# Kernel tuning notes

Hardware: AMD Instinct MI355X
Metric: run time of the kernel (lower is better)

## Reference

```python
import jax, jax.numpy as jnp
import numpy as np

RADIUS = 1.0


def setup_inputs() -> dict:
    key = jax.random.key(0)
    ks = jax.random.split(key, 9)
    Nq, No, P, L = 1024, 2048, 3, 64
    pos_query = jax.random.uniform(ks[0], (Nq, P), dtype=jnp.float32)
    pos_obs = jax.random.uniform(ks[1], (No, P), dtype=jnp.float32)
    h_obs = jax.random.normal(ks[2], (No, L), dtype=jnp.float32)
    # kernel_mlp: Linear(3*P, L) -> ReLU -> Linear(L, 1)
    W1 = jax.random.normal(ks[3], (3 * P, L), dtype=jnp.float32) * (1.0 / np.sqrt(3 * P))
    b1 = jnp.zeros((L,), jnp.float32)
    W2 = jax.random.normal(ks[4], (L, 1), dtype=jnp.float32) * (1.0 / np.sqrt(L))
    b2 = jnp.zeros((1,), jnp.float32)
    # value_proj: Linear(L, L)
    Wv = jax.random.normal(ks[5], (L, L), dtype=jnp.float32) * (1.0 / np.sqrt(L))
    bv = jnp.zeros((L,), jnp.float32)
    obs_mask = jnp.ones((No,), jnp.int32)
    obs_batch = jnp.sort(jax.random.randint(ks[6], (No,), 0, 4, dtype=jnp.int32))
    query_batch = jnp.sort(jax.random.randint(ks[7], (Nq,), 0, 4, dtype=jnp.int32))
    return dict(h_obs=h_obs, pos_obs=pos_obs, pos_query=pos_query,
                W1=W1, b1=b1, W2=W2, b2=b2, Wv=Wv, bv=bv,
                obs_mask=obs_mask, obs_batch=obs_batch, query_batch=query_batch)


def reference(h_obs, pos_obs, pos_query, W1, b1, W2, b2, Wv, bv,
              obs_mask, obs_batch, query_batch):
    Nq, P = pos_query.shape
    No = pos_obs.shape[0]
    rel = pos_query[:, None, :] - pos_obs[None, :, :]                 # [Nq,No,P]
    kin = jnp.concatenate([
        jnp.broadcast_to(pos_query[:, None, :], (Nq, No, P)),
        jnp.broadcast_to(pos_obs[None, :, :], (Nq, No, P)),
        rel,
    ], axis=-1)                                                        # [Nq,No,3P]
    hidden = jax.nn.relu(jnp.einsum('qop,pl->qol', kin, W1) + b1)      # [Nq,No,L]
    logits = jnp.einsum('qol,lk->qok', hidden, W2)[..., 0] + b2[0]     # [Nq,No]
    # masks: same batch, within radius, observed
    same = query_batch[:, None] == obs_batch[None, :]
    dist = jnp.linalg.norm(rel, axis=-1)
    mask = same & (dist <= RADIUS) & (obs_mask[None, :] != 0)
    # masked softmax over obs dim; fully-masked rows -> all-zero weights
    # (matches torch softmax(-inf row) -> nan -> nan_to_num(0))
    logits_safe = jnp.where(mask, logits, 0.0)
    m = jnp.max(jnp.where(mask, logits, -jnp.inf), axis=1, keepdims=True)
    m = jnp.where(jnp.isfinite(m), m, 0.0)
    e = jnp.where(mask, jnp.exp(logits_safe - m), 0.0)
    denom = jnp.sum(e, axis=1, keepdims=True)
    weights = e / jnp.maximum(denom, 1e-30)                            # [Nq,No]
    v = h_obs @ Wv + bv                                                # [No,L]
    return weights @ v                                                 # [Nq,L]
```

## Files before the change

### kernel.cpp

```cpp
#include <hip/hip_runtime.h>
#include <math.h>

#define LDIM 64
#define QT2 32
#define QW 8
#define QT3 4
#define SEG 4
#define LOG2E 1.4426950408889634f

static __device__ __forceinline__ float fast_exp2(float x) {
#if __has_builtin(__builtin_amdgcn_exp2f)
    return __builtin_amdgcn_exp2f(x);
#else
    return exp2f(x);
#endif
}

__global__ __launch_bounds__(256) void gano_pre(
    const float* __restrict__ h_obs, const float* __restrict__ pos_obs,
    const float* __restrict__ pos_query,
    const float* __restrict__ W1, const float* __restrict__ b1,
    const float* __restrict__ W2,
    const float* __restrict__ Wv, const float* __restrict__ bv,
    const int* __restrict__ obs_mask, const int* __restrict__ obs_batch,
    const int* __restrict__ query_batch,
    float4* __restrict__ Bi, float4* __restrict__ P4,
    float* __restrict__ V, float* __restrict__ A, float* __restrict__ w2s,
    int2* __restrict__ qrange,
    int No, int NoA, int Nq)
{
    const int gid = blockIdx.x * blockDim.x + threadIdx.x;
    if (gid >= NoA * LDIM) return;
    {
        const int o = gid >> 6, l = gid & 63;
        float vv = 0.0f;
        if (o < No) {
            vv = bv[l];
            #pragma unroll 8
            for (int k = 0; k < LDIM; ++k)
                vv = fmaf(h_obs[o * LDIM + k], Wv[k * LDIM + l], vv);
        }
        V[gid] = vv;
    }
    if (gid < NoA * 16) {
        const int o = gid & 63, g = (gid >> 6) & 15, c = gid >> 10;
        const int oo = (c << 6) + o;
        float4 r = make_float4(0.f, 0.f, 0.f, 0.f);
        if (oo < No) {
            const float px = pos_obs[oo*3+0], py = pos_obs[oo*3+1], pz = pos_obs[oo*3+2];
            float* rr = (float*)&r;
            #pragma unroll
            for (int j = 0; j < 4; ++j) {
                const int l = 4 * g + j;
                float bb = b1[l];
                bb = fmaf(px, W1[3*LDIM+l] - W1[6*LDIM+l], bb);
                bb = fmaf(py, W1[4*LDIM+l] - W1[7*LDIM+l], bb);
                bb = fmaf(pz, W1[5*LDIM+l] - W1[8*LDIM+l], bb);
                rr[j] = bb;
            }
        }
        Bi[gid] = r;
    }
    if (gid < Nq * LDIM) {
        const int q = gid >> 6, l = gid & 63;
        float a = pos_query[q*3+0] * (W1[0*LDIM+l] + W1[6*LDIM+l]);
        a = fmaf(pos_query[q*3+1], W1[1*LDIM+l] + W1[7*LDIM+l], a);
        a = fmaf(pos_query[q*3+2], W1[2*LDIM+l] + W1[8*LDIM+l], a);
        A[gid] = a;
    }
    if (gid < LDIM) w2s[gid] = W2[gid] * LOG2E;
    if (gid < NoA) {
        float4 pp = make_float4(0.f, 0.f, 0.f, 0.f);
        if (gid < No)
            pp = make_float4(pos_obs[gid*3+0], pos_obs[gid*3+1], pos_obs[gid*3+2],
                             obs_mask[gid] ? (float)(obs_batch[gid] + 1) : 0.0f);
        P4[gid] = pp;
    }
    if (gid < Nq) {
        const int b = query_batch[gid];
        int lo = 0, hi = No;
        while (lo < hi) { int mid = (lo + hi) >> 1; if (obs_batch[mid] < b) lo = mid + 1; else hi = mid; }
        const int s = lo;
        hi = No;
        while (lo < hi) { int mid = (lo + hi) >> 1; if (obs_batch[mid] < b + 1) lo = mid + 1; else hi = mid; }
        qrange[gid] = make_int2(s, lo);
    }
}

__global__ __launch_bounds__(256) void gano_logits(
    const float4* __restrict__ Bi, const float4* __restrict__ P4,
    const float* __restrict__ A, const float* __restrict__ w2s,
    const float* __restrict__ pos_query,
    const int* __restrict__ obs_batch, const int* __restrict__ query_batch,
    float* __restrict__ lg, int No, int NoA)
{
    const int c  = blockIdx.x;
    const int q0 = blockIdx.y * QT2;
    if ((c << 6) >= No) return;
    const int c_lo = obs_batch[c << 6];
    const int c_hi = obs_batch[min((c << 6) + 63, No - 1)];
    const int t_lo = query_batch[q0];
    const int t_hi = query_batch[q0 + QT2 - 1];
    if (c_lo > t_hi || c_hi < t_lo) return;

    __shared__ float4 a4[QT2][16];
    __shared__ float4 w2_4[16];
    __shared__ float4 qp4[QT2];

    const int tid = threadIdx.x;
    for (int i = tid; i < QT2 * 16; i += 256)
        a4[i >> 4][i & 15] = ((const float4*)A)[((size_t)(q0 + (i >> 4)) << 4) + (i & 15)];
    if (tid < 16) w2_4[tid] = ((const float4*)w2s)[tid];
    if (tid < QT2) {
        const int q = q0 + tid;
        qp4[tid] = make_float4(pos_query[q*3+0], pos_query[q*3+1], pos_query[q*3+2],
                               (float)(query_batch[q] + 1));
    }
    __syncthreads();

    const int lane = tid & 63, wid = tid >> 6;
    const float4 p = P4[(c << 6) + lane];
    const float4* Bc = Bi + ((size_t)c << 10) + lane;

    float lgq[QW];
    #pragma unroll
    for (int j = 0; j < QW; ++j) lgq[j] = 0.0f;

    #pragma unroll
    for (int g = 0; g < 16; ++g) {
        const float4 Bv = Bc[g << 6];
        const float4 w  = w2_4[g];
        #pragma unroll
        for (int j = 0; j < QW; ++j) {
            const float4 a = a4[wid * QW + j][g];
            lgq[j] = fmaf(fmaxf(a.x + Bv.x, 0.f), w.x, lgq[j]);
            lgq[j] = fmaf(fmaxf(a.y + Bv.y, 0.f), w.y, lgq[j]);
            lgq[j] = fmaf(fmaxf(a.z + Bv.z, 0.f), w.z, lgq[j]);
            lgq[j] = fmaf(fmaxf(a.w + Bv.w, 0.f), w.w, lgq[j]);
        }
    }

    float* lrow = lg + (size_t)(q0 + wid * QW) * NoA + (c << 6) + lane;
    #pragma unroll
    for (int j = 0; j < QW; ++j) {
        const float4 qp = qp4[wid * QW + j];
        const float dx = qp.x - p.x, dy = qp.y - p.y, dz = qp.z - p.z;
        const float d2 = fmaf(dz, dz, fmaf(dy, dy, dx * dx));
        const bool valid = (p.w == qp.w) & (d2 <= 1.0f);
        lrow[(size_t)j * NoA] = valid ? lgq[j] : -INFINITY;
    }
}

__global__ __launch_bounds__(256) void gano_pv(
    const float* __restrict__ lg, const float* __restrict__ V,
    const int2* __restrict__ qrange,
    float* __restrict__ partA, int NoA)
{
    const int grp = blockIdx.x >> 2;
    const int seg = blockIdx.x & 3;
    const int q0  = grp * QT3;
    const int tid = threadIdx.x, lane = tid & 63, wid = tid >> 6;

    __shared__ float sM[QT3], sD[QT3];
    __shared__ float4 e4[4][LDIM];
    __shared__ float sacc[4][QT3][LDIM];

    {
        const int q = q0 + wid;
        const int2 r = qrange[q];
        const float* row = lg + (size_t)q * NoA;
        float mx = -INFINITY;
        for (int o = r.x + lane; o < r.y; o += 64) mx = fmaxf(mx, row[o]);
        #pragma unroll
        for (int m = 32; m; m >>= 1) mx = fmaxf(mx, __shfl_xor(mx, m, 64));
        const float Mq = (mx == -INFINITY) ? 0.0f : mx;
        float sum = 0.0f;
        for (int o = r.x + lane; o < r.y; o += 64) sum += fast_exp2(row[o] - Mq);
        #pragma unroll
        for (int m = 32; m; m >>= 1) sum += __shfl_xor(sum, m, 64);
        if (lane == 0) { sM[wid] = Mq; sD[wid] = sum; }
    }
    __syncthreads();

    const float M0 = sM[0], M1 = sM[1], M2 = sM[2], M3 = sM[3];
    float acc0 = 0.f, acc1 = 0.f, acc2 = 0.f, acc3 = 0.f;

    const int s4 = qrange[q0].x;
    const int e4u = qrange[q0 + QT3 - 1].y;
    if (e4u > s4) {
        const int c0 = s4 >> 6, c1 = (e4u - 1) >> 6;
        const int nc = c1 - c0 + 1;
        const int cs = c0 + (nc * seg) / SEG;
        const int ce = c0 + (nc * (seg + 1)) / SEG;
        const float* r0 = lg + (size_t)(q0 + 0) * NoA;
        const float* r1 = lg + (size_t)(q0 + 1) * NoA;
        const float* r2 = lg + (size_t)(q0 + 2) * NoA;
        const float* r3 = lg + (size_t)(q0 + 3) * NoA;
        for (int c = cs + wid; c < ce; c += 4) {
            const int o = (c << 6) + lane;
            float4 ev;
            ev.x = fast_exp2(r0[o] - M0);
            ev.y = fast_exp2(r1[o] - M1);
            ev.z = fast_exp2(r2[o] - M2);
            ev.w = fast_exp2(r3[o] - M3);
            e4[wid][lane] = ev;
            const float* Vc = V + ((size_t)c << 12) + lane;
            #pragma unroll
            for (int oo = 0; oo < LDIM; ++oo) {
                const float4 e = e4[wid][oo];
                const float vv = Vc[oo << 6];
                acc0 = fmaf(e.x, vv, acc0);
                acc1 = fmaf(e.y, vv, acc1);
                acc2 = fmaf(e.z, vv, acc2);
                acc3 = fmaf(e.w, vv, acc3);
            }
        }
    }

    sacc[wid][0][lane] = acc0;
    sacc[wid][1][lane] = acc1;
    sacc[wid][2][lane] = acc2;
    sacc[wid][3][lane] = acc3;
    __syncthreads();

    {
        const int q = wid;
        const float a = (sacc[0][q][lane] + sacc[1][q][lane]) +
                        (sacc[2][q][lane] + sacc[3][q][lane]);
        const float rd = 1.0f / fmaxf(sD[q], 1e-30f);
        partA[(((size_t)(q0 + q)) * SEG + seg) * LDIM + lane] = a * rd;
    }
}

__global__ __launch_bounds__(256) void gano_merge(
    const float* __restrict__ partA, float* __restrict__ out, int n)
{
    const int gid = blockIdx.x * blockDim.x + threadIdx.x;
    if (gid >= n) return;
    const int q = gid >> 6, l = gid & 63;
    const float* p = partA + ((size_t)q * SEG) * LDIM + l;
    out[gid] = (p[0] + p[LDIM]) + (p[2 * LDIM] + p[3 * LDIM]);
}

extern "C" void kernel_launch(void* const* d_in, const int* in_sizes, int n_in,
                              void* d_out, int out_size, void* d_ws, size_t ws_size,
                              hipStream_t stream) {
    const float* h_obs     = (const float*)d_in[0];
    const float* pos_obs   = (const float*)d_in[1];
    const float* pos_query = (const float*)d_in[2];
    const float* W1        = (const float*)d_in[3];
    const float* b1        = (const float*)d_in[4];
    const float* W2        = (const float*)d_in[5];
    const float* Wv        = (const float*)d_in[7];
    const float* bv        = (const float*)d_in[8];
    const int* obs_mask    = (const int*)d_in[9];
    const int* obs_batch   = (const int*)d_in[10];
    const int* query_batch = (const int*)d_in[11];

    const int No  = in_sizes[1] / 3;
    const int Nq  = in_sizes[2] / 3;
    const int NoA = (No + 63) & ~63;
    const int nChunks = NoA / 64;

    float4* Bi  = (float4*)d_ws;
    float4* P4  = Bi + (size_t)NoA * 16;
    float*  V   = (float*)(P4 + NoA);
    float*  A   = V + (size_t)NoA * LDIM;
    float*  w2s = A + (size_t)Nq * LDIM;
    int2*   qr  = (int2*)(w2s + LDIM);
    float*  lgb = (float*)(qr + Nq);
    float*  pA  = lgb + (size_t)Nq * NoA;

    gano_pre<<<(NoA * LDIM + 255) / 256, 256, 0, stream>>>(
        h_obs, pos_obs, pos_query, W1, b1, W2, Wv, bv,
        obs_mask, obs_batch, query_batch,
        Bi, P4, V, A, w2s, qr, No, NoA, Nq);

    dim3 g2(nChunks, Nq / QT2);
    gano_logits<<<g2, 256, 0, stream>>>(Bi, P4, A, w2s, pos_query,
                                        obs_batch, query_batch, lgb, No, NoA);

    gano_pv<<<(Nq / QT3) * SEG, 256, 0, stream>>>(lgb, V, qr, pA, NoA);

    gano_merge<<<(Nq * LDIM + 255) / 256, 256, 0, stream>>>(pA, (float*)d_out, Nq * LDIM);
}
```

Baseline: 31.87 us.

## Compute per-chunk softmax max/sum in logits kernel and drop merge pass

The logits kernel now applies the mask, then computes a per-64-obs-chunk max and exp-sum for each query with wave shuffles. It stores the exponentials plus those chunk statistics instead of raw logits. The PV kernel merges the chunk statistics into a row max and denominator, and rescales the stored exponentials by a per-chunk factor. This removes the two full-row passes for max and sum and the separate merge kernel launch. In exchange, the 4-way segment split of PV is dropped, so far fewer blocks run, and the combine step assumes at most 64 chunks per query group.

```diff
diff --git a/kernel.cpp b/kernel.cpp
--- a/kernel.cpp
+++ b/kernel.cpp
@@ -5,7 +5,6 @@
 #define QT2 32
 #define QW 8
 #define QT3 4
-#define SEG 4
 #define LOG2E 1.4426950408889634f
 
 static __device__ __forceinline__ float fast_exp2(float x) {
@@ -92,16 +91,15 @@
     const float* __restrict__ A, const float* __restrict__ w2s,
     const float* __restrict__ pos_query,
     const int* __restrict__ obs_batch, const int* __restrict__ query_batch,
-    float* __restrict__ lg, int No, int NoA)
+    float* __restrict__ ec, float* __restrict__ cmax, float* __restrict__ csum,
+    int No, int NoA, int nC)
 {
     const int c  = blockIdx.x;
     const int q0 = blockIdx.y * QT2;
     if ((c << 6) >= No) return;
     const int c_lo = obs_batch[c << 6];
     const int c_hi = obs_batch[min((c << 6) + 63, No - 1)];
-    const int t_lo = query_batch[q0];
-    const int t_hi = query_batch[q0 + QT2 - 1];
-    if (c_lo > t_hi || c_hi < t_lo) return;
+    if (c_lo > query_batch[q0 + QT2 - 1] || c_hi < query_batch[q0]) return;
 
     __shared__ float4 a4[QT2][16];
     __shared__ float4 w2_4[16];
@@ -140,70 +138,102 @@
         }
     }
 
-    float* lrow = lg + (size_t)(q0 + wid * QW) * NoA + (c << 6) + lane;
     #pragma unroll
     for (int j = 0; j < QW; ++j) {
         const float4 qp = qp4[wid * QW + j];
         const float dx = qp.x - p.x, dy = qp.y - p.y, dz = qp.z - p.z;
         const float d2 = fmaf(dz, dz, fmaf(dy, dy, dx * dx));
         const bool valid = (p.w == qp.w) & (d2 <= 1.0f);
-        lrow[(size_t)j * NoA] = valid ? lgq[j] : -INFINITY;
+        lgq[j] = valid ? lgq[j] : -INFINITY;
+    }
+
+    float mc[QW];
+    #pragma unroll
+    for (int j = 0; j < QW; ++j) mc[j] = lgq[j];
+    #pragma unroll
+    for (int msk = 32; msk; msk >>= 1) {
+        #pragma unroll
+        for (int j = 0; j < QW; ++j) mc[j] = fmaxf(mc[j], __shfl_xor(mc[j], msk, 64));
+    }
+    float ev[QW], sc[QW];
+    #pragma unroll
+    for (int j = 0; j < QW; ++j) {
+        ev[j] = (mc[j] == -INFINITY) ? 0.0f : fast_exp2(lgq[j] - mc[j]);
+        sc[j] = ev[j];
+    }
+    #pragma unroll
+    for (int msk = 32; msk; msk >>= 1) {
+        #pragma unroll
+        for (int j = 0; j < QW; ++j) sc[j] += __shfl_xor(sc[j], msk, 64);
+    }
+
+    float* erow = ec + (size_t)(q0 + wid * QW) * NoA + (c << 6) + lane;
+    #pragma unroll
+    for (int j = 0; j < QW; ++j) erow[(size_t)j * NoA] = ev[j];
+    if (lane == 0) {
+        #pragma unroll
+        for (int j = 0; j < QW; ++j) {
+            const int q = q0 + wid * QW + j;
+            cmax[(size_t)q * nC + c] = mc[j];
+            csum[(size_t)q * nC + c] = sc[j];
+        }
     }
 }
 
 __global__ __launch_bounds__(256) void gano_pv(
-    const float* __restrict__ lg, const float* __restrict__ V,
+    const float* __restrict__ ec, const float* __restrict__ V,
+    const float* __restrict__ cmax, const float* __restrict__ csum,
     const int2* __restrict__ qrange,
-    float* __restrict__ partA, int NoA)
+    float* __restrict__ out, int NoA, int nC)
 {
-    const int grp = blockIdx.x >> 2;
-    const int seg = blockIdx.x & 3;
-    const int q0  = grp * QT3;
+    const int q0  = blockIdx.x * QT3;
     const int tid = threadIdx.x, lane = tid & 63, wid = tid >> 6;
 
-    __shared__ float sM[QT3], sD[QT3];
+    __shared__ float sD[QT3];
+    __shared__ float sScale[QT3][64];
     __shared__ float4 e4[4][LDIM];
     __shared__ float sacc[4][QT3][LDIM];
 
+    const int s4  = qrange[q0].x;
+    const int e4u = qrange[q0 + QT3 - 1].y;
+    const int c0  = s4 >> 6;
+    const int c1  = (e4u > s4) ? ((e4u - 1) >> 6) : (c0 - 1);
+    const int nc  = c1 - c0 + 1;
+
     {
         const int q = q0 + wid;
-        const int2 r = qrange[q];
-        const float* row = lg + (size_t)q * NoA;
-        float mx = -INFINITY;
-        for (int o = r.x + lane; o < r.y; o += 64) mx = fmaxf(mx, row[o]);
+        const bool on = (lane < nc);
+        const float mcv = on ? cmax[(size_t)q * nC + c0 + lane] : -INFINITY;
+        const float scv = on ? csum[(size_t)q * nC + c0 + lane] : 0.0f;
+        float mx = mcv;
         #pragma unroll
         for (int m = 32; m; m >>= 1) mx = fmaxf(mx, __shfl_xor(mx, m, 64));
         const float Mq = (mx == -INFINITY) ? 0.0f : mx;
-        float sum = 0.0f;
-        for (int o = r.x + lane; o < r.y; o += 64) sum += fast_exp2(row[o] - Mq);
-        #pragma unroll
-        for (int m = 32; m; m >>= 1) sum += __shfl_xor(sum, m, 64);
-        if (lane == 0) { sM[wid] = Mq; sD[wid] = sum; }
+        const float scale = (mcv == -INFINITY) ? 0.0f : fast_exp2(mcv - Mq);
+        float d = scv * scale;
+        #pragma unroll
+        for (int m = 32; m; m >>= 1) d += __shfl_xor(d, m, 64);
+        if (on) sScale[wid][lane] = scale;
+        if (lane == 0) sD[wid] = d;
     }
     __syncthreads();
 
-    const float M0 = sM[0], M1 = sM[1], M2 = sM[2], M3 = sM[3];
     float acc0 = 0.f, acc1 = 0.f, acc2 = 0.f, acc3 = 0.f;
 
-    const int s4 = qrange[q0].x;
-    const int e4u = qrange[q0 + QT3 - 1].y;
-    if (e4u > s4) {
-        const int c0 = s4 >> 6, c1 = (e4u - 1) >> 6;
-        const int nc = c1 - c0 + 1;
-        const int cs = c0 + (nc * seg) / SEG;
-        const int ce = c0 + (nc * (seg + 1)) / SEG;
-        const float* r0 = lg + (size_t)(q0 + 0) * NoA;
-        const float* r1 = lg + (size_t)(q0 + 1) * NoA;
-        const float* r2 = lg + (size_t)(q0 + 2) * NoA;
-        const float* r3 = lg + (size_t)(q0 + 3) * NoA;
-        for (int c = cs + wid; c < ce; c += 4) {
+    if (nc > 0) {
+        const float* r0 = ec + (size_t)(q0 + 0) * NoA;
+        const float* r1 = ec + (size_t)(q0 + 1) * NoA;
+        const float* r2 = ec + (size_t)(q0 + 2) * NoA;
+        const float* r3 = ec + (size_t)(q0 + 3) * NoA;
+        for (int c = c0 + wid; c <= c1; c += 4) {
             const int o = (c << 6) + lane;
-            float4 ev;
-            ev.x = fast_exp2(r0[o] - M0);
-            ev.y = fast_exp2(r1[o] - M1);
-            ev.z = fast_exp2(r2[o] - M2);
-            ev.w = fast_exp2(r3[o] - M3);
-            e4[wid][lane] = ev;
+            const int ci = c - c0;
+            float4 evv;
+            evv.x = r0[o] * sScale[0][ci];
+            evv.y = r1[o] * sScale[1][ci];
+            evv.z = r2[o] * sScale[2][ci];
+            evv.w = r3[o] * sScale[3][ci];
+            e4[wid][lane] = evv;
             const float* Vc = V + ((size_t)c << 12) + lane;
             #pragma unroll
             for (int oo = 0; oo < LDIM; ++oo) {
@@ -227,19 +257,8 @@
         const int q = wid;
         const float a = (sacc[0][q][lane] + sacc[1][q][lane]) +
                         (sacc[2][q][lane] + sacc[3][q][lane]);
-        const float rd = 1.0f / fmaxf(sD[q], 1e-30f);
-        partA[(((size_t)(q0 + q)) * SEG + seg) * LDIM + lane] = a * rd;
-    }
-}
-
-__global__ __launch_bounds__(256) void gano_merge(
-    const float* __restrict__ partA, float* __restrict__ out, int n)
-{
-    const int gid = blockIdx.x * blockDim.x + threadIdx.x;
-    if (gid >= n) return;
-    const int q = gid >> 6, l = gid & 63;
-    const float* p = partA + ((size_t)q * SEG) * LDIM + l;
-    out[gid] = (p[0] + p[LDIM]) + (p[2 * LDIM] + p[3 * LDIM]);
+        out[(size_t)(q0 + q) * LDIM + lane] = a / fmaxf(sD[q], 1e-30f);
+    }
 }
 
 extern "C" void kernel_launch(void* const* d_in, const int* in_sizes, int n_in,
@@ -260,27 +279,28 @@
     const int No  = in_sizes[1] / 3;
     const int Nq  = in_sizes[2] / 3;
     const int NoA = (No + 63) & ~63;
-    const int nChunks = NoA / 64;
-
-    float4* Bi  = (float4*)d_ws;
-    float4* P4  = Bi + (size_t)NoA * 16;
-    float*  V   = (float*)(P4 + NoA);
-    float*  A   = V + (size_t)NoA * LDIM;
-    float*  w2s = A + (size_t)Nq * LDIM;
-    int2*   qr  = (int2*)(w2s + LDIM);
-    float*  lgb = (float*)(qr + Nq);
-    float*  pA  = lgb + (size_t)Nq * NoA;
+    const int nC  = NoA / 64;
+
+    float4* Bi   = (float4*)d_ws;
+    float4* P4   = Bi + (size_t)NoA * 16;
+    float*  V    = (float*)(P4 + NoA);
+    float*  A    = V + (size_t)NoA * LDIM;
+    float*  w2s  = A + (size_t)Nq * LDIM;
+    int2*   qr   = (int2*)(w2s + LDIM);
+    float*  ecb  = (float*)(qr + Nq);
+    float*  cmax = ecb + (size_t)Nq * NoA;
+    float*  csum = cmax + (size_t)Nq * nC;
 
     gano_pre<<<(NoA * LDIM + 255) / 256, 256, 0, stream>>>(
         h_obs, pos_obs, pos_query, W1, b1, W2, Wv, bv,
         obs_mask, obs_batch, query_batch,
         Bi, P4, V, A, w2s, qr, No, NoA, Nq);
 
-    dim3 g2(nChunks, Nq / QT2);
+    dim3 g2(nC, Nq / QT2);
     gano_logits<<<g2, 256, 0, stream>>>(Bi, P4, A, w2s, pos_query,
-                                        obs_batch, query_batch, lgb, No, NoA);
-
-    gano_pv<<<(Nq / QT3) * SEG, 256, 0, stream>>>(lgb, V, qr, pA, NoA);
-
-    gano_merge<<<(Nq * LDIM + 255) / 256, 256, 0, stream>>>(pA, (float*)d_out, Nq * LDIM);
-}
+                                        obs_batch, query_batch,
+                                        ecb, cmax, csum, No, NoA, nC);
+
+    gano_pv<<<Nq / QT3, 256, 0, stream>>>(ecb, V, cmax, csum, qr,
+                                          (float*)d_out, NoA, nC);
+}
```

Measured after the change: 34.64 us. 1.09x slower.

## Fuse logits, masked softmax and value aggregation into one kernel

Applied to the files above, without the earlier changes.

Replaces the logits, PV and merge kernels with one fused kernel. Each 512-thread block takes four queries, recomputes the MLP logits for the obs chunks in its batch range, applies the mask and exp, and accumulates both the weighted V sum and the denominator in one pass. This removes the Nq×No logits buffer round trip, the separate max and sum passes, the partial-sum merge and two launches. In exchange it drops the max subtraction before exp, so large logits could overflow, and per-query work now runs on fewer, larger blocks.

```diff
diff --git a/kernel.cpp b/kernel.cpp
--- a/kernel.cpp
+++ b/kernel.cpp
@@ -2,10 +2,9 @@
 #include <math.h>
 
 #define LDIM 64
-#define QT2 32
-#define QW 8
-#define QT3 4
-#define SEG 4
+#define QT 4
+#define TPB 512
+#define NWAVE 8
 #define LOG2E 1.4426950408889634f
 
 static __device__ __forceinline__ float fast_exp2(float x) {
@@ -18,16 +17,11 @@
 
 __global__ __launch_bounds__(256) void gano_pre(
     const float* __restrict__ h_obs, const float* __restrict__ pos_obs,
-    const float* __restrict__ pos_query,
     const float* __restrict__ W1, const float* __restrict__ b1,
-    const float* __restrict__ W2,
     const float* __restrict__ Wv, const float* __restrict__ bv,
     const int* __restrict__ obs_mask, const int* __restrict__ obs_batch,
-    const int* __restrict__ query_batch,
-    float4* __restrict__ Bi, float4* __restrict__ P4,
-    float* __restrict__ V, float* __restrict__ A, float* __restrict__ w2s,
-    int2* __restrict__ qrange,
-    int No, int NoA, int Nq)
+    float4* __restrict__ Bi, float4* __restrict__ P4, float* __restrict__ V,
+    int No, int NoA)
 {
     const int gid = blockIdx.x * blockDim.x + threadIdx.x;
     if (gid >= NoA * LDIM) return;
@@ -36,7 +30,7 @@
         float vv = 0.0f;
         if (o < No) {
             vv = bv[l];
-            #pragma unroll 8
+            #pragma unroll 16
             for (int k = 0; k < LDIM; ++k)
                 vv = fmaf(h_obs[o * LDIM + k], Wv[k * LDIM + l], vv);
         }
@@ -61,14 +55,6 @@
         }
         Bi[gid] = r;
     }
-    if (gid < Nq * LDIM) {
-        const int q = gid >> 6, l = gid & 63;
-        float a = pos_query[q*3+0] * (W1[0*LDIM+l] + W1[6*LDIM+l]);
-        a = fmaf(pos_query[q*3+1], W1[1*LDIM+l] + W1[7*LDIM+l], a);
-        a = fmaf(pos_query[q*3+2], W1[2*LDIM+l] + W1[8*LDIM+l], a);
-        A[gid] = a;
-    }
-    if (gid < LDIM) w2s[gid] = W2[gid] * LOG2E;
     if (gid < NoA) {
         float4 pp = make_float4(0.f, 0.f, 0.f, 0.f);
         if (gid < No)
@@ -76,134 +62,113 @@
                              obs_mask[gid] ? (float)(obs_batch[gid] + 1) : 0.0f);
         P4[gid] = pp;
     }
-    if (gid < Nq) {
-        const int b = query_batch[gid];
+}
+
+__global__ __launch_bounds__(TPB) void gano_fused(
+    const float4* __restrict__ Bi, const float4* __restrict__ P4,
+    const float* __restrict__ V,
+    const float* __restrict__ pos_query, const float* __restrict__ W1,
+    const float* __restrict__ W2,
+    const int* __restrict__ obs_batch, const int* __restrict__ query_batch,
+    float* __restrict__ out, int No, int Nq)
+{
+    const int q0   = blockIdx.x * QT;
+    const int tid  = threadIdx.x;
+    const int lane = tid & 63;
+    const int wid  = tid >> 6;
+
+    __shared__ float4 a4[16][QT];
+    __shared__ float4 w2_4[16];
+    __shared__ float4 qp4[QT];
+    __shared__ int2   srange;
+    __shared__ float4 e4[NWAVE][LDIM];
+    __shared__ float  sacc[NWAVE][QT][LDIM];
+    __shared__ float  sden[NWAVE][QT];
+
+    if (tid < QT * LDIM) {
+        const int q = tid >> 6, l = tid & 63;
+        const int qq = min(q0 + q, Nq - 1);
+        float a = pos_query[qq*3+0] * (W1[0*LDIM+l] + W1[6*LDIM+l]);
+        a = fmaf(pos_query[qq*3+1], W1[1*LDIM+l] + W1[7*LDIM+l], a);
+        a = fmaf(pos_query[qq*3+2], W1[2*LDIM+l] + W1[8*LDIM+l], a);
+        ((float*)&a4[l >> 2][q])[l & 3] = a;
+        if (q == 0) ((float*)w2_4)[l] = W2[l] * LOG2E;
+    }
+    if (tid < QT) {
+        const int qq = min(q0 + tid, Nq - 1);
+        qp4[tid] = make_float4(pos_query[qq*3+0], pos_query[qq*3+1], pos_query[qq*3+2],
+                               (float)(query_batch[qq] + 1));
+    }
+    if (tid == TPB - 1) {
+        const int b_lo = query_batch[q0];
+        const int b_hi = query_batch[min(q0 + QT - 1, Nq - 1)];
         int lo = 0, hi = No;
-        while (lo < hi) { int mid = (lo + hi) >> 1; if (obs_batch[mid] < b) lo = mid + 1; else hi = mid; }
+        while (lo < hi) { int mid = (lo + hi) >> 1; if (obs_batch[mid] < b_lo) lo = mid + 1; else hi = mid; }
         const int s = lo;
         hi = No;
-        while (lo < hi) { int mid = (lo + hi) >> 1; if (obs_batch[mid] < b + 1) lo = mid + 1; else hi = mid; }
-        qrange[gid] = make_int2(s, lo);
-    }
-}
-
-__global__ __launch_bounds__(256) void gano_logits(
-    const float4* __restrict__ Bi, const float4* __restrict__ P4,
-    const float* __restrict__ A, const float* __restrict__ w2s,
-    const float* __restrict__ pos_query,
-    const int* __restrict__ obs_batch, const int* __restrict__ query_batch,
-    float* __restrict__ lg, int No, int NoA)
-{
-    const int c  = blockIdx.x;
-    const int q0 = blockIdx.y * QT2;
-    if ((c << 6) >= No) return;
-    const int c_lo = obs_batch[c << 6];
-    const int c_hi = obs_batch[min((c << 6) + 63, No - 1)];
-    const int t_lo = query_batch[q0];
-    const int t_hi = query_batch[q0 + QT2 - 1];
-    if (c_lo > t_hi || c_hi < t_lo) return;
-
-    __shared__ float4 a4[QT2][16];
-    __shared__ float4 w2_4[16];
-    __shared__ float4 qp4[QT2];
-
-    const int tid = threadIdx.x;
-    for (int i = tid; i < QT2 * 16; i += 256)
-        a4[i >> 4][i & 15] = ((const float4*)A)[((size_t)(q0 + (i >> 4)) << 4) + (i & 15)];
-    if (tid < 16) w2_4[tid] = ((const float4*)w2s)[tid];
-    if (tid < QT2) {
-        const int q = q0 + tid;
-        qp4[tid] = make_float4(pos_query[q*3+0], pos_query[q*3+1], pos_query[q*3+2],
-                               (float)(query_batch[q] + 1));
+        while (lo < hi) { int mid = (lo + hi) >> 1; if (obs_batch[mid] < b_hi + 1) lo = mid + 1; else hi = mid; }
+        srange = make_int2(s, lo);
     }
     __syncthreads();
 
-    const int lane = tid & 63, wid = tid >> 6;
-    const float4 p = P4[(c << 6) + lane];
-    const float4* Bc = Bi + ((size_t)c << 10) + lane;
-
-    float lgq[QW];
-    #pragma unroll
-    for (int j = 0; j < QW; ++j) lgq[j] = 0.0f;
-
-    #pragma unroll
-    for (int g = 0; g < 16; ++g) {
-        const float4 Bv = Bc[g << 6];
-        const float4 w  = w2_4[g];
-        #pragma unroll
-        for (int j = 0; j < QW; ++j) {
-            const float4 a = a4[wid * QW + j][g];
-            lgq[j] = fmaf(fmaxf(a.x + Bv.x, 0.f), w.x, lgq[j]);
-            lgq[j] = fmaf(fmaxf(a.y + Bv.y, 0.f), w.y, lgq[j]);
-            lgq[j] = fmaf(fmaxf(a.z + Bv.z, 0.f), w.z, lgq[j]);
-            lgq[j] = fmaf(fmaxf(a.w + Bv.w, 0.f), w.w, lgq[j]);
-        }
-    }
-
-    float* lrow = lg + (size_t)(q0 + wid * QW) * NoA + (c << 6) + lane;
-    #pragma unroll
-    for (int j = 0; j < QW; ++j) {
-        const float4 qp = qp4[wid * QW + j];
-        const float dx = qp.x - p.x, dy = qp.y - p.y, dz = qp.z - p.z;
-        const float d2 = fmaf(dz, dz, fmaf(dy, dy, dx * dx));
-        const bool valid = (p.w == qp.w) & (d2 <= 1.0f);
-        lrow[(size_t)j * NoA] = valid ? lgq[j] : -INFINITY;
-    }
-}
-
-__global__ __launch_bounds__(256) void gano_pv(
-    const float* __restrict__ lg, const float* __restrict__ V,
-    const int2* __restrict__ qrange,
-    float* __restrict__ partA, int NoA)
-{
-    const int grp = blockIdx.x >> 2;
-    const int seg = blockIdx.x & 3;
-    const int q0  = grp * QT3;
-    const int tid = threadIdx.x, lane = tid & 63, wid = tid >> 6;
-
-    __shared__ float sM[QT3], sD[QT3];
-    __shared__ float4 e4[4][LDIM];
-    __shared__ float sacc[4][QT3][LDIM];
-
-    {
-        const int q = q0 + wid;
-        const int2 r = qrange[q];
-        const float* row = lg + (size_t)q * NoA;
-        float mx = -INFINITY;
-        for (int o = r.x + lane; o < r.y; o += 64) mx = fmaxf(mx, row[o]);
-        #pragma unroll
-        for (int m = 32; m; m >>= 1) mx = fmaxf(mx, __shfl_xor(mx, m, 64));
-        const float Mq = (mx == -INFINITY) ? 0.0f : mx;
-        float sum = 0.0f;
-        for (int o = r.x + lane; o < r.y; o += 64) sum += fast_exp2(row[o] - Mq);
-        #pragma unroll
-        for (int m = 32; m; m >>= 1) sum += __shfl_xor(sum, m, 64);
-        if (lane == 0) { sM[wid] = Mq; sD[wid] = sum; }
-    }
-    __syncthreads();
-
-    const float M0 = sM[0], M1 = sM[1], M2 = sM[2], M3 = sM[3];
+    const int start = srange.x, end = srange.y;
+    float d0 = 0.f, d1 = 0.f, d2_ = 0.f, d3 = 0.f;
     float acc0 = 0.f, acc1 = 0.f, acc2 = 0.f, acc3 = 0.f;
 
-    const int s4 = qrange[q0].x;
-    const int e4u = qrange[q0 + QT3 - 1].y;
-    if (e4u > s4) {
-        const int c0 = s4 >> 6, c1 = (e4u - 1) >> 6;
-        const int nc = c1 - c0 + 1;
-        const int cs = c0 + (nc * seg) / SEG;
-        const int ce = c0 + (nc * (seg + 1)) / SEG;
-        const float* r0 = lg + (size_t)(q0 + 0) * NoA;
-        const float* r1 = lg + (size_t)(q0 + 1) * NoA;
-        const float* r2 = lg + (size_t)(q0 + 2) * NoA;
-        const float* r3 = lg + (size_t)(q0 + 3) * NoA;
-        for (int c = cs + wid; c < ce; c += 4) {
+    if (end > start) {
+        const int c0 = start >> 6, c1 = (end - 1) >> 6;
+        for (int c = c0 + wid; c <= c1; c += NWAVE) {
             const int o = (c << 6) + lane;
+            const float4 p = P4[o];
+            const float4* Bc = Bi + ((size_t)c << 10) + lane;
+
+            float lg0 = 0.f, lg1 = 0.f, lg2 = 0.f, lg3 = 0.f;
+            #pragma unroll
+            for (int g = 0; g < 16; ++g) {
+                const float4 Bv = Bc[g << 6];
+                const float4 w  = w2_4[g];
+                const float4 A0 = a4[g][0], A1 = a4[g][1], A2 = a4[g][2], A3 = a4[g][3];
+                lg0 = fmaf(fmaxf(A0.x + Bv.x, 0.f), w.x, lg0);
+                lg1 = fmaf(fmaxf(A1.x + Bv.x, 0.f), w.x, lg1);
+                lg2 = fmaf(fmaxf(A2.x + Bv.x, 0.f), w.x, lg2);
+                lg3 = fmaf(fmaxf(A3.x + Bv.x, 0.f), w.x, lg3);
+                lg0 = fmaf(fmaxf(A0.y + Bv.y, 0.f), w.y, lg0);
+                lg1 = fmaf(fmaxf(A1.y + Bv.y, 0.f), w.y, lg1);
+                lg2 = fmaf(fmaxf(A2.y + Bv.y, 0.f), w.y, lg2);
+                lg3 = fmaf(fmaxf(A3.y + Bv.y, 0.f), w.y, lg3);
+                lg0 = fmaf(fmaxf(A0.z + Bv.z, 0.f), w.z, lg0);
+                lg1 = fmaf(fmaxf(A1.z + Bv.z, 0.f), w.z, lg1);
+                lg2 = fmaf(fmaxf(A2.z + Bv.z, 0.f), w.z, lg2);
+                lg3 = fmaf(fmaxf(A3.z + Bv.z, 0.f), w.z, lg3);
+                lg0 = fmaf(fmaxf(A0.w + Bv.w, 0.f), w.w, lg0);
+                lg1 = fmaf(fmaxf(A1.w + Bv.w, 0.f), w.w, lg1);
+                lg2 = fmaf(fmaxf(A2.w + Bv.w, 0.f), w.w, lg2);
+                lg3 = fmaf(fmaxf(A3.w + Bv.w, 0.f), w.w, lg3);
+            }
+
             float4 ev;
-            ev.x = fast_exp2(r0[o] - M0);
-            ev.y = fast_exp2(r1[o] - M1);
-            ev.z = fast_exp2(r2[o] - M2);
-            ev.w = fast_exp2(r3[o] - M3);
+            {
+                float4 qp;
+                qp = qp4[0];
+                { const float dx=qp.x-p.x, dy=qp.y-p.y, dz=qp.z-p.z;
+                  const float dd=fmaf(dz,dz,fmaf(dy,dy,dx*dx));
+                  ev.x = ((p.w==qp.w)&(dd<=1.0f)) ? fast_exp2(lg0) : 0.0f; }
+                qp = qp4[1];
+                { const float dx=qp.x-p.x, dy=qp.y-p.y, dz=qp.z-p.z;
+                  const float dd=fmaf(dz,dz,fmaf(dy,dy,dx*dx));
+                  ev.y = ((p.w==qp.w)&(dd<=1.0f)) ? fast_exp2(lg1) : 0.0f; }
+                qp = qp4[2];
+                { const float dx=qp.x-p.x, dy=qp.y-p.y, dz=qp.z-p.z;
+                  const float dd=fmaf(dz,dz,fmaf(dy,dy,dx*dx));
+                  ev.z = ((p.w==qp.w)&(dd<=1.0f)) ? fast_exp2(lg2) : 0.0f; }
+                qp = qp4[3];
+                { const float dx=qp.x-p.x, dy=qp.y-p.y, dz=qp.z-p.z;
+                  const float dd=fmaf(dz,dz,fmaf(dy,dy,dx*dx));
+                  ev.w = ((p.w==qp.w)&(dd<=1.0f)) ? fast_exp2(lg3) : 0.0f; }
+            }
+            d0 += ev.x; d1 += ev.y; d2_ += ev.z; d3 += ev.w;
             e4[wid][lane] = ev;
+
             const float* Vc = V + ((size_t)c << 12) + lane;
             #pragma unroll
             for (int oo = 0; oo < LDIM; ++oo) {
@@ -217,29 +182,33 @@
         }
     }
 
+    #pragma unroll
+    for (int msk = 32; msk; msk >>= 1) {
+        d0 += __shfl_xor(d0, msk, 64);
+        d1 += __shfl_xor(d1, msk, 64);
+        d2_ += __shfl_xor(d2_, msk, 64);
+        d3 += __shfl_xor(d3, msk, 64);
+    }
+    if (lane == 0) {
+        sden[wid][0] = d0; sden[wid][1] = d1; sden[wid][2] = d2_; sden[wid][3] = d3;
+    }
     sacc[wid][0][lane] = acc0;
     sacc[wid][1][lane] = acc1;
     sacc[wid][2][lane] = acc2;
     sacc[wid][3][lane] = acc3;
     __syncthreads();
 
-    {
+    if (wid < QT) {
         const int q = wid;
-        const float a = (sacc[0][q][lane] + sacc[1][q][lane]) +
-                        (sacc[2][q][lane] + sacc[3][q][lane]);
-        const float rd = 1.0f / fmaxf(sD[q], 1e-30f);
-        partA[(((size_t)(q0 + q)) * SEG + seg) * LDIM + lane] = a * rd;
-    }
-}
-
-__global__ __launch_bounds__(256) void gano_merge(
-    const float* __restrict__ partA, float* __restrict__ out, int n)
-{
-    const int gid = blockIdx.x * blockDim.x + threadIdx.x;
-    if (gid >= n) return;
-    const int q = gid >> 6, l = gid & 63;
-    const float* p = partA + ((size_t)q * SEG) * LDIM + l;
-    out[gid] = (p[0] + p[LDIM]) + (p[2 * LDIM] + p[3 * LDIM]);
+        float A = 0.f, D = 0.f;
+        #pragma unroll
+        for (int w = 0; w < NWAVE; ++w) {
+            A += sacc[w][q][lane];
+            D += sden[w][q];
+        }
+        if (q0 + q < Nq)
+            out[(size_t)(q0 + q) * LDIM + lane] = A / fmaxf(D, 1e-30f);
+    }
 }
 
 extern "C" void kernel_launch(void* const* d_in, const int* in_sizes, int n_in,
@@ -260,27 +229,16 @@
     const int No  = in_sizes[1] / 3;
     const int Nq  = in_sizes[2] / 3;
     const int NoA = (No + 63) & ~63;
-    const int nChunks = NoA / 64;
-
-    float4* Bi  = (float4*)d_ws;
-    float4* P4  = Bi + (size_t)NoA * 16;
-    float*  V   = (float*)(P4 + NoA);
-    float*  A   = V + (size_t)NoA * LDIM;
-    float*  w2s = A + (size_t)Nq * LDIM;
-    int2*   qr  = (int2*)(w2s + LDIM);
-    float*  lgb = (float*)(qr + Nq);
-    float*  pA  = lgb + (size_t)Nq * NoA;
+
+    float4* Bi = (float4*)d_ws;
+    float4* P4 = Bi + (size_t)NoA * 16;
+    float*  V  = (float*)(P4 + NoA);
 
     gano_pre<<<(NoA * LDIM + 255) / 256, 256, 0, stream>>>(
-        h_obs, pos_obs, pos_query, W1, b1, W2, Wv, bv,
-        obs_mask, obs_batch, query_batch,
-        Bi, P4, V, A, w2s, qr, No, NoA, Nq);
-
-    dim3 g2(nChunks, Nq / QT2);
-    gano_logits<<<g2, 256, 0, stream>>>(Bi, P4, A, w2s, pos_query,
-                                        obs_batch, query_batch, lgb, No, NoA);
-
-    gano_pv<<<(Nq / QT3) * SEG, 256, 0, stream>>>(lgb, V, qr, pA, NoA);
-
-    gano_merge<<<(Nq * LDIM + 255) / 256, 256, 0, stream>>>(pA, (float*)d_out, Nq * LDIM);
-}
+        h_obs, pos_obs, W1, b1, Wv, bv, obs_mask, obs_batch,
+        Bi, P4, V, No, NoA);
+
+    gano_fused<<<(Nq + QT - 1) / QT, TPB, 0, stream>>>(
+        Bi, P4, V, pos_query, W1, W2, obs_batch, query_batch,
+        (float*)d_out, No, Nq);
+}
```

Measured after the change: 56.86 us. 1.78x slower.

## Fuse logits, softmax and PV into one kernel with atomic accumulation

Applied to the files above, without the earlier changes.

Merges the logits, softmax/PV and merge kernels into one accumulate kernel. Each block exponentiates its masked logits, stages them in LDS, multiplies by its V chunk, and atomically adds partial numerators and denominators. A small normalize kernel then divides. This removes the full Nq x No logits buffer round-trip, the per-query range search and two launches. In exchange it drops the max-subtraction in the softmax, which risks overflow for large logits, and adds float atomics with nondeterministic summation order. It also raises the unroll factor in the V projection loop.

```diff
diff --git a/kernel.cpp b/kernel.cpp
--- a/kernel.cpp
+++ b/kernel.cpp
@@ -4,8 +4,6 @@
 #define LDIM 64
 #define QT2 32
 #define QW 8
-#define QT3 4
-#define SEG 4
 #define LOG2E 1.4426950408889634f
 
 static __device__ __forceinline__ float fast_exp2(float x) {
@@ -23,10 +21,8 @@
     const float* __restrict__ W2,
     const float* __restrict__ Wv, const float* __restrict__ bv,
     const int* __restrict__ obs_mask, const int* __restrict__ obs_batch,
-    const int* __restrict__ query_batch,
-    float4* __restrict__ Bi, float4* __restrict__ P4,
-    float* __restrict__ V, float* __restrict__ A, float* __restrict__ w2s,
-    int2* __restrict__ qrange,
+    float4* __restrict__ Bi, float4* __restrict__ P4, float* __restrict__ V,
+    float* __restrict__ A, float* __restrict__ w2s, float* __restrict__ zeroRegion,
     int No, int NoA, int Nq)
 {
     const int gid = blockIdx.x * blockDim.x + threadIdx.x;
@@ -36,7 +32,7 @@
         float vv = 0.0f;
         if (o < No) {
             vv = bv[l];
-            #pragma unroll 8
+            #pragma unroll 16
             for (int k = 0; k < LDIM; ++k)
                 vv = fmaf(h_obs[o * LDIM + k], Wv[k * LDIM + l], vv);
         }
@@ -76,36 +72,28 @@
                              obs_mask[gid] ? (float)(obs_batch[gid] + 1) : 0.0f);
         P4[gid] = pp;
     }
-    if (gid < Nq) {
-        const int b = query_batch[gid];
-        int lo = 0, hi = No;
-        while (lo < hi) { int mid = (lo + hi) >> 1; if (obs_batch[mid] < b) lo = mid + 1; else hi = mid; }
-        const int s = lo;
-        hi = No;
-        while (lo < hi) { int mid = (lo + hi) >> 1; if (obs_batch[mid] < b + 1) lo = mid + 1; else hi = mid; }
-        qrange[gid] = make_int2(s, lo);
-    }
-}
-
-__global__ __launch_bounds__(256) void gano_logits(
+    if (gid < Nq * (LDIM + 1)) zeroRegion[gid] = 0.0f;
+}
+
+__global__ __launch_bounds__(256) void gano_accum(
     const float4* __restrict__ Bi, const float4* __restrict__ P4,
-    const float* __restrict__ A, const float* __restrict__ w2s,
-    const float* __restrict__ pos_query,
+    const float* __restrict__ V, const float* __restrict__ A,
+    const float* __restrict__ w2s, const float* __restrict__ pos_query,
     const int* __restrict__ obs_batch, const int* __restrict__ query_batch,
-    float* __restrict__ lg, int No, int NoA)
+    float* __restrict__ acc, float* __restrict__ den,
+    int No, int Nq)
 {
     const int c  = blockIdx.x;
     const int q0 = blockIdx.y * QT2;
     if ((c << 6) >= No) return;
     const int c_lo = obs_batch[c << 6];
     const int c_hi = obs_batch[min((c << 6) + 63, No - 1)];
-    const int t_lo = query_batch[q0];
-    const int t_hi = query_batch[q0 + QT2 - 1];
-    if (c_lo > t_hi || c_hi < t_lo) return;
+    if (c_lo > query_batch[q0 + QT2 - 1] || c_hi < query_batch[q0]) return;
 
     __shared__ float4 a4[QT2][16];
     __shared__ float4 w2_4[16];
     __shared__ float4 qp4[QT2];
+    __shared__ float  e_lds[QT2][LDIM];
 
     const int tid = threadIdx.x;
     for (int i = tid; i < QT2 * 16; i += 256)
@@ -125,7 +113,6 @@
     float lgq[QW];
     #pragma unroll
     for (int j = 0; j < QW; ++j) lgq[j] = 0.0f;
-
     #pragma unroll
     for (int g = 0; g < 16; ++g) {
         const float4 Bv = Bc[g << 6];
@@ -140,106 +127,57 @@
         }
     }
 
-    float* lrow = lg + (size_t)(q0 + wid * QW) * NoA + (c << 6) + lane;
+    float ds[QW];
     #pragma unroll
     for (int j = 0; j < QW; ++j) {
         const float4 qp = qp4[wid * QW + j];
         const float dx = qp.x - p.x, dy = qp.y - p.y, dz = qp.z - p.z;
         const float d2 = fmaf(dz, dz, fmaf(dy, dy, dx * dx));
         const bool valid = (p.w == qp.w) & (d2 <= 1.0f);
-        lrow[(size_t)j * NoA] = valid ? lgq[j] : -INFINITY;
-    }
-}
-
-__global__ __launch_bounds__(256) void gano_pv(
-    const float* __restrict__ lg, const float* __restrict__ V,
-    const int2* __restrict__ qrange,
-    float* __restrict__ partA, int NoA)
-{
-    const int grp = blockIdx.x >> 2;
-    const int seg = blockIdx.x & 3;
-    const int q0  = grp * QT3;
-    const int tid = threadIdx.x, lane = tid & 63, wid = tid >> 6;
-
-    __shared__ float sM[QT3], sD[QT3];
-    __shared__ float4 e4[4][LDIM];
-    __shared__ float sacc[4][QT3][LDIM];
-
-    {
-        const int q = q0 + wid;
-        const int2 r = qrange[q];
-        const float* row = lg + (size_t)q * NoA;
-        float mx = -INFINITY;
-        for (int o = r.x + lane; o < r.y; o += 64) mx = fmaxf(mx, row[o]);
-        #pragma unroll
-        for (int m = 32; m; m >>= 1) mx = fmaxf(mx, __shfl_xor(mx, m, 64));
-        const float Mq = (mx == -INFINITY) ? 0.0f : mx;
-        float sum = 0.0f;
-        for (int o = r.x + lane; o < r.y; o += 64) sum += fast_exp2(row[o] - Mq);
-        #pragma unroll
-        for (int m = 32; m; m >>= 1) sum += __shfl_xor(sum, m, 64);
-        if (lane == 0) { sM[wid] = Mq; sD[wid] = sum; }
-    }
-    __syncthreads();
-
-    const float M0 = sM[0], M1 = sM[1], M2 = sM[2], M3 = sM[3];
-    float acc0 = 0.f, acc1 = 0.f, acc2 = 0.f, acc3 = 0.f;
-
-    const int s4 = qrange[q0].x;
-    const int e4u = qrange[q0 + QT3 - 1].y;
-    if (e4u > s4) {
-        const int c0 = s4 >> 6, c1 = (e4u - 1) >> 6;
-        const int nc = c1 - c0 + 1;
-        const int cs = c0 + (nc * seg) / SEG;
-        const int ce = c0 + (nc * (seg + 1)) / SEG;
-        const float* r0 = lg + (size_t)(q0 + 0) * NoA;
-        const float* r1 = lg + (size_t)(q0 + 1) * NoA;
-        const float* r2 = lg + (size_t)(q0 + 2) * NoA;
-        const float* r3 = lg + (size_t)(q0 + 3) * NoA;
-        for (int c = cs + wid; c < ce; c += 4) {
-            const int o = (c << 6) + lane;
-            float4 ev;
-            ev.x = fast_exp2(r0[o] - M0);
-            ev.y = fast_exp2(r1[o] - M1);
-            ev.z = fast_exp2(r2[o] - M2);
-            ev.w = fast_exp2(r3[o] - M3);
-            e4[wid][lane] = ev;
-            const float* Vc = V + ((size_t)c << 12) + lane;
-            #pragma unroll
-            for (int oo = 0; oo < LDIM; ++oo) {
-                const float4 e = e4[wid][oo];
-                const float vv = Vc[oo << 6];
-                acc0 = fmaf(e.x, vv, acc0);
-                acc1 = fmaf(e.y, vv, acc1);
-                acc2 = fmaf(e.z, vv, acc2);
-                acc3 = fmaf(e.w, vv, acc3);
-            }
-        }
-    }
-
-    sacc[wid][0][lane] = acc0;
-    sacc[wid][1][lane] = acc1;
-    sacc[wid][2][lane] = acc2;
-    sacc[wid][3][lane] = acc3;
-    __syncthreads();
-
-    {
-        const int q = wid;
-        const float a = (sacc[0][q][lane] + sacc[1][q][lane]) +
-                        (sacc[2][q][lane] + sacc[3][q][lane]);
-        const float rd = 1.0f / fmaxf(sD[q], 1e-30f);
-        partA[(((size_t)(q0 + q)) * SEG + seg) * LDIM + lane] = a * rd;
-    }
-}
-
-__global__ __launch_bounds__(256) void gano_merge(
-    const float* __restrict__ partA, float* __restrict__ out, int n)
+        const float e = valid ? fast_exp2(lgq[j]) : 0.0f;
+        e_lds[wid * QW + j][lane] = e;
+        ds[j] = e;
+    }
+    #pragma unroll
+    for (int msk = 32; msk; msk >>= 1) {
+        #pragma unroll
+        for (int j = 0; j < QW; ++j) ds[j] += __shfl_xor(ds[j], msk, 64);
+    }
+    if (lane == 0) {
+        #pragma unroll
+        for (int j = 0; j < QW; ++j) atomicAdd(&den[q0 + wid * QW + j], ds[j]);
+    }
+
+    const float* Vc = V + ((size_t)c << 12) + lane;
+    float pacc[QW];
+    #pragma unroll
+    for (int j = 0; j < QW; ++j) pacc[j] = 0.0f;
+    for (int oo = 0; oo < LDIM; oo += 4) {
+        const float v0 = Vc[(oo + 0) << 6];
+        const float v1 = Vc[(oo + 1) << 6];
+        const float v2 = Vc[(oo + 2) << 6];
+        const float v3 = Vc[(oo + 3) << 6];
+        #pragma unroll
+        for (int j = 0; j < QW; ++j) {
+            const float4 e = *(const float4*)&e_lds[wid * QW + j][oo];
+            pacc[j] = fmaf(e.x, v0, pacc[j]);
+            pacc[j] = fmaf(e.y, v1, pacc[j]);
+            pacc[j] = fmaf(e.z, v2, pacc[j]);
+            pacc[j] = fmaf(e.w, v3, pacc[j]);
+        }
+    }
+    #pragma unroll
+    for (int j = 0; j < QW; ++j)
+        atomicAdd(&acc[(size_t)(q0 + wid * QW + j) * LDIM + lane], pacc[j]);
+}
+
+__global__ __launch_bounds__(256) void gano_norm(
+    const float* __restrict__ acc, const float* __restrict__ den,
+    float* __restrict__ out, int n)
 {
     const int gid = blockIdx.x * blockDim.x + threadIdx.x;
     if (gid >= n) return;
-    const int q = gid >> 6, l = gid & 63;
-    const float* p = partA + ((size_t)q * SEG) * LDIM + l;
-    out[gid] = (p[0] + p[LDIM]) + (p[2 * LDIM] + p[3 * LDIM]);
+    out[gid] = acc[gid] / fmaxf(den[gid >> 6], 1e-30f);
 }
 
 extern "C" void kernel_launch(void* const* d_in, const int* in_sizes, int n_in,
@@ -260,27 +198,23 @@
     const int No  = in_sizes[1] / 3;
     const int Nq  = in_sizes[2] / 3;
     const int NoA = (No + 63) & ~63;
-    const int nChunks = NoA / 64;
+    const int nC  = NoA / 64;
 
     float4* Bi  = (float4*)d_ws;
     float4* P4  = Bi + (size_t)NoA * 16;
     float*  V   = (float*)(P4 + NoA);
     float*  A   = V + (size_t)NoA * LDIM;
     float*  w2s = A + (size_t)Nq * LDIM;
-    int2*   qr  = (int2*)(w2s + LDIM);
-    float*  lgb = (float*)(qr + Nq);
-    float*  pA  = lgb + (size_t)Nq * NoA;
+    float*  acc = w2s + LDIM;
+    float*  den = acc + (size_t)Nq * LDIM;
 
     gano_pre<<<(NoA * LDIM + 255) / 256, 256, 0, stream>>>(
-        h_obs, pos_obs, pos_query, W1, b1, W2, Wv, bv,
-        obs_mask, obs_batch, query_batch,
-        Bi, P4, V, A, w2s, qr, No, NoA, Nq);
-
-    dim3 g2(nChunks, Nq / QT2);
-    gano_logits<<<g2, 256, 0, stream>>>(Bi, P4, A, w2s, pos_query,
-                                        obs_batch, query_batch, lgb, No, NoA);
-
-    gano_pv<<<(Nq / QT3) * SEG, 256, 0, stream>>>(lgb, V, qr, pA, NoA);
-
-    gano_merge<<<(Nq * LDIM + 255) / 256, 256, 0, stream>>>(pA, (float*)d_out, Nq * LDIM);
-}
+        h_obs, pos_obs, pos_query, W1, b1, W2, Wv, bv, obs_mask, obs_batch,
+        Bi, P4, V, A, w2s, acc, No, NoA, Nq);
+
+    dim3 g2(nC, Nq / QT2);
+    gano_accum<<<g2, 256, 0, stream>>>(Bi, P4, V, A, w2s, pos_query,
+                                       obs_batch, query_batch, acc, den, No, Nq);
+
+    gano_norm<<<(Nq * LDIM + 255) / 256, 256, 0, stream>>>(acc, den, (float*)d_out, Nq * LDIM);
+}
```

Result: faster. 29.04 us (-8.9%).
